# Performance work log

Hardware: AMD Instinct MI355X
Metric: run time of the kernel (lower is better)

## Reference

```python
import jax, jax.numpy as jnp
import numpy as np

N, D_IN, D_OUT, N_CTRS, K = 16384, 64, 64, 512, 16


def setup_inputs() -> dict:
    key = jax.random.key(0)
    k1, k2, k3, k4 = jax.random.split(key, 4)
    x = jax.random.normal(k1, (N, D_IN), dtype=jnp.float32)
    ctrs = jax.random.normal(k2, (N_CTRS, D_IN), dtype=jnp.float32)
    Wv = jax.random.normal(k3, (N_CTRS, D_IN, D_OUT), dtype=jnp.float32) * 0.02
    Ov = jax.random.normal(k4, (N_CTRS, D_OUT), dtype=jnp.float32) * 0.02
    return {"x": x, "ctrs": ctrs, "Wv": Wv, "Ov": Ov, "k": K}


def reference(x, ctrs, Wv, Ov, k):
    n = x.shape[0]
    # squared distances via expansion (same math as sum((x-c)^2), avoids [n,C,d] blowup)
    x2 = jnp.sum(x * x, axis=1, keepdims=True)            # [n,1]
    c2 = jnp.sum(ctrs * ctrs, axis=1)                     # [C]
    dist_sq = x2 + c2[None, :] - 2.0 * (x @ ctrs.T)       # [n,C]
    # k nearest centers; softmax over negative squared distances of the k selected
    neg_top, idx = jax.lax.top_k(-dist_sq, k)             # [n,k] each
    scores = jax.nn.softmax(neg_top, axis=1)              # [n,k]
    # dense soft-assignment matrix (only k nonzeros per row), as in the torch code
    A = jnp.zeros_like(dist_sq).at[jnp.arange(n)[:, None], idx].set(scores)  # [n,C]
    # per-token affine mix: sum_c A[n,c] * (x[n] @ Wv[c] + Ov[c])
    scored_weights = jnp.einsum('nc,cgp->ngp', A, Wv)     # [n,d_in,d_out]
    out = jnp.einsum('ngp,ng->np', scored_weights, x) + A @ Ov  # [n,d_out]
    return out
```

## Files before the change

kernel.cpp:

```cpp
#include <hip/hip_runtime.h>
#include <hip/hip_fp16.h>

#define N_TOK 16384
#define D 64
#define NC 512
#define KSEL 16
#define NPAIR (N_TOK * KSEL)
#define PADCAP 327168

typedef __attribute__((ext_vector_type(8))) short short8;
typedef __attribute__((ext_vector_type(8))) unsigned short ushort8;
typedef __attribute__((ext_vector_type(16))) float float16;

__device__ __forceinline__ unsigned fkey(float f) {
    unsigned u = __float_as_uint(f);
    return (u & 0x80000000u) ? ~u : (u | 0x80000000u);
}
__device__ __forceinline__ float funkey(unsigned k) {
    unsigned u = (k & 0x80000000u) ? (k & 0x7fffffffu) : ~k;
    return __uint_as_float(u);
}
__device__ __forceinline__ unsigned short bfr(float f) {
    unsigned u = __float_as_uint(f);
    return (unsigned short)((u + 0x7FFFu + ((u >> 16) & 1u)) >> 16);
}
__device__ __forceinline__ float b2f(unsigned short h) {
    return __uint_as_float((unsigned)h << 16);
}

__device__ __forceinline__ void ins16(unsigned (&run)[16], unsigned k) {
    #pragma unroll
    for (int r = 0; r < 16; ++r) {
        unsigned mx = run[r] > k ? run[r] : k;
        unsigned mn = run[r] > k ? k : run[r];
        run[r] = mx; k = mn;
    }
}

__global__ __launch_bounds__(256) void prep2_kernel(
    const float* __restrict__ x, const float* __restrict__ ctrs,
    const float* __restrict__ Wv,
    unsigned short* __restrict__ xh, unsigned short* __restrict__ xl,
    unsigned short* __restrict__ cbf, float* __restrict__ c2g,
    unsigned short* __restrict__ wbt, int* __restrict__ tokentab,
    int* __restrict__ hist) {
    __shared__ unsigned short tw[64 * 68];
    const int b = blockIdx.x, t = threadIdx.x;
    if (b < 512) {
        int g = b * 256 + t;
        int row = g >> 3, seg = g & 7;
        const float4* xp = (const float4*)(x + row * 64 + seg * 8);
        float4 u = xp[0], v = xp[1];
        float c[8] = {u.x, u.y, u.z, u.w, v.x, v.y, v.z, v.w};
        ushort8 h, l;
        #pragma unroll
        for (int j = 0; j < 8; ++j) {
            h[j] = bfr(c[j]);
            l[j] = bfr(c[j] - b2f(h[j]));
        }
        *(ushort8*)(xh + row * 64 + seg * 8) = h;
        *(ushort8*)(xl + row * 64 + seg * 8) = l;
    } else if (b < 516) {
        int g = (b - 512) * 256 + t;
        int c = g >> 1, q = g & 1;
        const float4* cp = (const float4*)(ctrs + c * D + q * 32);
        unsigned short* Ch = cbf + c * 136 + q * 32;
        float s2 = 0.f;
        #pragma unroll
        for (int i = 0; i < 8; ++i) {
            float4 v = cp[i];
            s2 += v.x * v.x + v.y * v.y + v.z * v.z + v.w * v.w;
            unsigned short h0 = bfr(v.x), h1 = bfr(v.y), h2 = bfr(v.z), h3 = bfr(v.w);
            unsigned short l0 = bfr(v.x - b2f(h0)), l1 = bfr(v.y - b2f(h1));
            unsigned short l2 = bfr(v.z - b2f(h2)), l3 = bfr(v.w - b2f(h3));
            *(uint2*)(Ch + 4 * i) =
                make_uint2((unsigned)h0 | ((unsigned)h1 << 16),
                           (unsigned)h2 | ((unsigned)h3 << 16));
            *(uint2*)(Ch + 64 + 4 * i) =
                make_uint2((unsigned)l0 | ((unsigned)l1 << 16),
                           (unsigned)l2 | ((unsigned)l3 << 16));
        }
        s2 += __shfl_xor(s2, 1);
        c2g[c] = s2;
    } else if (b < 1028) {
        const float* Wp = Wv + (size_t)(b - 516) * 4096;
        #pragma unroll
        for (int i = 0; i < 16; ++i) {
            int e = t + 256 * i;
            tw[(e & 63) * 68 + (e >> 6)] = bfr(Wp[e]);
        }
        __syncthreads();
        unsigned short* Wo = wbt + (size_t)(b - 516) * 4096;
        #pragma unroll
        for (int i = 0; i < 2; ++i) {
            int idx8 = t + 256 * i;
            int p = idx8 >> 3, g0 = (idx8 & 7) * 8;
            ushort8 v;
            #pragma unroll
            for (int j = 0; j < 8; ++j) v[j] = tw[p * 68 + g0 + j];
            *(ushort8*)(Wo + idx8 * 8) = v;
        }
    } else if (b < 1348) {
        int i = (b - 1028) * 256 + t;
        if (i < PADCAP / 4) ((int4*)tokentab)[i] = make_int4(-1, -1, -1, -1);
    } else {
        hist[t] = 0; hist[t + 256] = 0; hist[t + 512] = 0; hist[t + 768] = 0;
    }
}

__global__ __launch_bounds__(256, 4) void topk15_kernel(
    const unsigned short* __restrict__ xh, const unsigned short* __restrict__ xl,
    const unsigned short* __restrict__ cbf, const float* __restrict__ c2g,
    unsigned* __restrict__ pk) {
    __shared__ __align__(16) unsigned char pool[35328];
    unsigned short* Cbf = (unsigned short*)pool;
    unsigned* Sbk = (unsigned*)pool;
    unsigned* mbp = (unsigned*)pool;
    float* c2s = (float*)(pool + 34816);

    const int t = threadIdx.x;
    const int lane = t & 63;
    const int wv = t >> 6;
    const int mrow = lane & 31;
    const int half = lane >> 5;
    const int tb = blockIdx.x >> 2;
    const int p = blockIdx.x & 3;
    const int base = tb * 64;
    const int cbase = p * 128;
    const int trow = (wv & 1) * 32;
    const int cgrp = (wv >> 1) * 64;

    {
        const uint4* src = (const uint4*)(cbf + (size_t)cbase * 136);
        uint4* dst = (uint4*)pool;
        #pragma unroll
        for (int i = 0; i < 8; ++i) dst[t + 256 * i] = src[t + 256 * i];
        if (t < 128) {
            dst[2048 + t] = src[2048 + t];
            c2s[t] = c2g[cbase + t];
        }
    }

    short8 ah[4], al[4];
    {
        const int xrow = base + trow + mrow;
        const unsigned short* xph = xh + (size_t)xrow * 64 + half * 8;
        const unsigned short* xpl = xl + (size_t)xrow * 64 + half * 8;
        #pragma unroll
        for (int kt = 0; kt < 4; ++kt) {
            ah[kt] = *(const short8*)(xph + kt * 16);
            al[kt] = *(const short8*)(xpl + kt * 16);
        }
    }
    __syncthreads();

    float16 acc0 = {0.f,0.f,0.f,0.f,0.f,0.f,0.f,0.f,0.f,0.f,0.f,0.f,0.f,0.f,0.f,0.f};
    float16 acc1 = acc0;

    const unsigned short* B0 = Cbf + (cgrp + mrow) * 136 + half * 8;
    const unsigned short* B1 = Cbf + (cgrp + 32 + mrow) * 136 + half * 8;
    #pragma unroll
    for (int kt = 0; kt < 4; ++kt) {
        short8 bh0 = *(const short8*)(B0 + kt * 16);
        short8 bh1 = *(const short8*)(B1 + kt * 16);
        short8 bl0 = *(const short8*)(B0 + 64 + kt * 16);
        short8 bl1 = *(const short8*)(B1 + 64 + kt * 16);
        acc0 = __builtin_amdgcn_mfma_f32_32x32x16_bf16(ah[kt], bh0, acc0, 0, 0, 0);
        acc1 = __builtin_amdgcn_mfma_f32_32x32x16_bf16(ah[kt], bh1, acc1, 0, 0, 0);
        acc0 = __builtin_amdgcn_mfma_f32_32x32x16_bf16(al[kt], bh0, acc0, 0, 0, 0);
        acc1 = __builtin_amdgcn_mfma_f32_32x32x16_bf16(al[kt], bh1, acc1, 0, 0, 0);
        acc0 = __builtin_amdgcn_mfma_f32_32x32x16_bf16(ah[kt], bl0, acc0, 0, 0, 0);
        acc1 = __builtin_amdgcn_mfma_f32_32x32x16_bf16(ah[kt], bl1, acc1, 0, 0, 0);
    }
    __syncthreads();

    {
        float ca = c2s[cgrp + mrow];
        float cb = c2s[cgrp + 32 + mrow];
        #pragma unroll
        for (int reg = 0; reg < 16; ++reg) {
            int tokrow = trow + (reg & 3) + 8 * (reg >> 2) + 4 * half;
            float sa = fmaf(2.f, acc0[reg], -ca);
            float sb = fmaf(2.f, acc1[reg], -cb);
            Sbk[tokrow * 132 + cgrp + mrow] =
                (fkey(sa) & 0xFFFFFE00u) | (unsigned)(cbase + cgrp + mrow);
            Sbk[tokrow * 132 + cgrp + 32 + mrow] =
                (fkey(sb) & 0xFFFFFE00u) | (unsigned)(cbase + cgrp + 32 + mrow);
        }
    }
    __syncthreads();

    const int tok = t & 63;
    const int h = t >> 6;
    unsigned run[16];
    #pragma unroll
    for (int r = 0; r < 16; ++r) run[r] = 0u;
    #pragma unroll
    for (int i = 0; i < 8; ++i) {
        int cq = ((i + tok) & 7) ^ ((tok >> 3) & 7);
        uint4 kv = *(const uint4*)(Sbk + tok * 132 + 32 * h + 4 * cq);
        ins16(run, kv.x); ins16(run, kv.y); ins16(run, kv.z); ins16(run, kv.w);
    }
    __syncthreads();

    {
        uint4* dst = (uint4*)(mbp + tok * 68 + h * 16);
        dst[0] = make_uint4(run[0], run[1], run[2], run[3]);
        dst[1] = make_uint4(run[4], run[5], run[6], run[7]);
        dst[2] = make_uint4(run[8], run[9], run[10], run[11]);
        dst[3] = make_uint4(run[12], run[13], run[14], run[15]);
    }
    __syncthreads();

    if (t < 64) {
        const unsigned* pm = mbp + t * 68;
        unsigned hv[4]; int pos[4];
        #pragma unroll
        for (int w = 0; w < 4; ++w) { pos[w] = 0; hv[w] = pm[w * 16]; }
        unsigned mm[16];
        #pragma unroll
        for (int r = 0; r < 16; ++r) {
            unsigned m = hv[0];
            #pragma unroll
            for (int w = 1; w < 4; ++w) m = m > hv[w] ? m : hv[w];
            mm[r] = m;
            #pragma unroll
            for (int w = 0; w < 4; ++w) {
                if (hv[w] == m) {
                    ++pos[w];
                    hv[w] = (pos[w] < 16) ? pm[w * 16 + pos[w]] : 0u;
                }
            }
        }
        uint4* dst = (uint4*)(pk + (size_t)(base + t) * 64 + p * 16);
        dst[0] = make_uint4(mm[0], mm[1], mm[2], mm[3]);
        dst[1] = make_uint4(mm[4], mm[5], mm[6], mm[7]);
        dst[2] = make_uint4(mm[8], mm[9], mm[10], mm[11]);
        dst[3] = make_uint4(mm[12], mm[13], mm[14], mm[15]);
    }
}

__global__ __launch_bounds__(256) void topmerge_kernel(
    const unsigned* __restrict__ pk, float* __restrict__ scores,
    int* __restrict__ sidx, int* __restrict__ hist) {
    __shared__ int lhist[NC];
    const int t = threadIdx.x;
    lhist[t] = 0; lhist[t + 256] = 0;
    __syncthreads();
    const int n = blockIdx.x * 256 + t;
    const unsigned* p = pk + (size_t)n * 64;
    unsigned h[4]; int pos[4];
    #pragma unroll
    for (int w = 0; w < 4; ++w) { pos[w] = 0; h[w] = p[w * 16]; }
    float vals[16]; int ids[16];
    #pragma unroll
    for (int r = 0; r < KSEL; ++r) {
        unsigned m = h[0];
        #pragma unroll
        for (int w = 1; w < 4; ++w) m = m > h[w] ? m : h[w];
        vals[r] = funkey(m);
        ids[r] = (int)(m & 511u);
        #pragma unroll
        for (int w = 0; w < 4; ++w) {
            if (h[w] == m) {
                ++pos[w];
                h[w] = (pos[w] < KSEL) ? p[w * 16 + pos[w]] : 0u;
            }
        }
    }
    float mx = vals[0];
    float e[16]; float sum = 0.f;
    #pragma unroll
    for (int r = 0; r < KSEL; ++r) { e[r] = __expf(vals[r] - mx); sum += e[r]; }
    float inv = 1.f / sum;
    #pragma unroll
    for (int q = 0; q < 4; ++q) {
        *(float4*)(scores + n * KSEL + 4 * q) =
            make_float4(e[4*q] * inv, e[4*q+1] * inv, e[4*q+2] * inv, e[4*q+3] * inv);
        *(int4*)(sidx + n * KSEL + 4 * q) =
            make_int4(ids[4*q], ids[4*q+1], ids[4*q+2], ids[4*q+3]);
    }
    #pragma unroll
    for (int r = 0; r < KSEL; ++r) atomicAdd(&lhist[ids[r]], 1);
    __syncthreads();
    { int hv = lhist[t]; if (hv) atomicAdd(&hist[t], hv); }
    { int hv = lhist[t + 256]; if (hv) atomicAdd(&hist[t + 256], hv); }
}

__global__ __launch_bounds__(256) void scatter5_kernel(
    const int* __restrict__ hist, const int* __restrict__ sidx,
    const float* __restrict__ scores, int* __restrict__ cursor,
    int* __restrict__ tokentab, float* __restrict__ scotab,
    int* __restrict__ meta) {
    __shared__ int buf[2][NC];
    __shared__ int sb[NC];
    __shared__ int lh[NC];
    __shared__ int lbase[NC];
    const int t = threadIdx.x;

    int h0 = hist[t], h1 = hist[t + 256];
    int p0 = (h0 + 127) & ~127, p1 = (h1 + 127) & ~127;
    buf[0][t] = p0; buf[0][t + 256] = p1;
    __syncthreads();
    int a = 0;
    for (int d = 1; d < NC; d <<= 1) {
        int v0 = buf[a][t] + (t >= d ? buf[a][t - d] : 0);
        int v1 = buf[a][t + 256] + (t + 256 >= d ? buf[a][t + 256 - d] : 0);
        buf[1 - a][t] = v0; buf[1 - a][t + 256] = v1;
        __syncthreads();
        a ^= 1;
    }
    sb[t] = buf[a][t] - p0;
    sb[t + 256] = buf[a][t + 256] - p1;
    if (t == 255) meta[0] = buf[a][NC - 1];
    lh[t] = 0; lh[t + 256] = 0;
    __syncthreads();

    const int base_e = blockIdx.x * 1024;
    int myc[4];
    #pragma unroll
    for (int i = 0; i < 4; ++i) {
        int c = sidx[base_e + t + 256 * i];
        myc[i] = c;
        atomicAdd(&lh[c], 1);
    }
    __syncthreads();
    for (int i = t; i < NC; i += 256) {
        int h = lh[i];
        lbase[i] = h ? (sb[i] + atomicAdd(&cursor[i], h)) : 0;
        lh[i] = 0;
    }
    __syncthreads();
    #pragma unroll
    for (int i = 0; i < 4; ++i) {
        int e = base_e + t + 256 * i;
        int c = myc[i];
        int pos = lbase[c] + atomicAdd(&lh[c], 1);
        tokentab[pos] = (c << 19) | e;
        scotab[pos] = scores[e];
    }
}

__global__ __launch_bounds__(256) void mix17_kernel(
    const unsigned short* __restrict__ xh, const unsigned short* __restrict__ wbt,
    const float* __restrict__ Ov, const int* __restrict__ tokentab,
    const float* __restrict__ scotab, const int* __restrict__ meta,
    __half* __restrict__ partial) {
    __shared__ __align__(16) unsigned short Wt[64 * 72];
    __shared__ int eT[128];
    __shared__ float sT[128];

    const int t = threadIdx.x;
    const int base = blockIdx.x * 128;
    if (base >= meta[0]) return;

    const int c = (int)(((unsigned)tokentab[base]) >> 19);

    {
        const unsigned short* Wp = wbt + (size_t)c * 4096;
        const int p = t >> 2, qq = t & 3;
        *(ushort8*)(Wt + p * 72 + qq * 16) =
            *(const ushort8*)(Wp + p * 64 + qq * 16);
        *(ushort8*)(Wt + p * 72 + qq * 16 + 8) =
            *(const ushort8*)(Wp + p * 64 + qq * 16 + 8);
    }
    if (t < 128) {
        unsigned w = (unsigned)tokentab[base + t];
        eT[t] = (int)(w & 0x7FFFFu);
        sT[t] = scotab[base + t];
    }
    __syncthreads();

    const int lane = t & 63;
    const int wv = t >> 6;
    const int mrow = lane & 31;
    const int half = lane >> 5;
    const int row = wv * 32 + mrow;

    const int mye = eT[row];
    const int myn = (mye < NPAIR) ? (mye >> 4) : 0;

    const unsigned short* xp = xh + (size_t)myn * 64 + half * 8;
    short8 a[4];
    #pragma unroll
    for (int kt = 0; kt < 4; ++kt) a[kt] = *(const short8*)(xp + kt * 16);

    float16 acc0 = {0.f,0.f,0.f,0.f,0.f,0.f,0.f,0.f,0.f,0.f,0.f,0.f,0.f,0.f,0.f,0.f};
    float16 acc1 = {0.f,0.f,0.f,0.f,0.f,0.f,0.f,0.f,0.f,0.f,0.f,0.f,0.f,0.f,0.f,0.f};

    const unsigned short* B0 = Wt + mrow * 72;
    const unsigned short* B1 = Wt + (mrow + 32) * 72;
    #pragma unroll
    for (int kt = 0; kt < 4; ++kt) {
        short8 b0 = *(const short8*)(B0 + kt * 16 + half * 8);
        short8 b1 = *(const short8*)(B1 + kt * 16 + half * 8);
        acc0 = __builtin_amdgcn_mfma_f32_32x32x16_bf16(a[kt], b0, acc0, 0, 0, 0);
        acc1 = __builtin_amdgcn_mfma_f32_32x32x16_bf16(a[kt], b1, acc1, 0, 0, 0);
    }

    const float ov0 = Ov[c * D + mrow];
    const float ov1 = Ov[c * D + 32 + mrow];
    #pragma unroll
    for (int reg = 0; reg < 16; ++reg) {
        int orow = wv * 32 + (reg & 3) + 8 * (reg >> 2) + 4 * half;
        float s = sT[orow];
        int e = eT[orow];
        if (e < NPAIR) {
            __half* dst = partial + (size_t)e * D;
            dst[mrow]      = __float2half(s * (acc0[reg] + ov0));
            dst[32 + mrow] = __float2half(s * (acc1[reg] + ov1));
        }
    }
}

__global__ __launch_bounds__(256) void redu2_kernel(
    const __half* __restrict__ partial, float* __restrict__ out) {
    const int g = blockIdx.x * 256 + threadIdx.x;
    const int n = g >> 3;
    const int d8 = (g & 7) * 8;
    const __half* p = partial + (size_t)n * (KSEL * D) + d8;
    float s[8] = {0.f, 0.f, 0.f, 0.f, 0.f, 0.f, 0.f, 0.f};
    #pragma unroll
    for (int r = 0; r < KSEL; ++r) {
        ushort8 v = *(const ushort8*)(p + r * D);
        #pragma unroll
        for (int j = 0; j < 8; ++j)
            s[j] += __half2float(__ushort_as_half((unsigned short)v[j]));
    }
    float* o = out + n * D + d8;
    *(float4*)(o)     = make_float4(s[0], s[1], s[2], s[3]);
    *(float4*)(o + 4) = make_float4(s[4], s[5], s[6], s[7]);
}

__global__ __launch_bounds__(256) void mix14_kernel(
    const float* __restrict__ x, const float* __restrict__ Wv,
    const float* __restrict__ Ov, const int* __restrict__ tokentab,
    const float* __restrict__ scotab, const int* __restrict__ meta,
    float* __restrict__ out) {
    __shared__ __align__(16) unsigned short Wt[64 * 72];
    __shared__ int tT[128];
    __shared__ float sT[128];

    const int t = threadIdx.x;
    const int base = blockIdx.x * 128;
    if (base >= meta[0]) return;

    const int c = (int)(((unsigned)tokentab[base]) >> 19);

    {
        const float* Wp = Wv + c * (D * D) + (t & 63);
        const int gb = (t >> 6) * 16;
        #pragma unroll
        for (int g = 0; g < 16; g += 2) {
            float v0 = Wp[(gb + g) * 64];
            float v1 = Wp[(gb + g + 1) * 64];
            unsigned pkw = (unsigned)bfr(v0) | ((unsigned)bfr(v1) << 16);
            *(unsigned*)&Wt[(t & 63) * 72 + gb + g] = pkw;
        }
    }
    if (t < 128) {
        unsigned w = (unsigned)tokentab[base + t];
        tT[t] = (int)((w & 0x7FFFFu) >> 4);
        sT[t] = scotab[base + t];
    }
    __syncthreads();

    const int lane = t & 63;
    const int wv = t >> 6;
    const int mrow = lane & 31;
    const int half = lane >> 5;
    const int row = wv * 32 + mrow;

    const int   myn = tT[row];
    const float mys = sT[row];

    const float* xp = x + myn * D + half * 8;
    float4 f[8];
    #pragma unroll
    for (int kt = 0; kt < 4; ++kt) {
        f[2 * kt]     = *(const float4*)(xp + kt * 16);
        f[2 * kt + 1] = *(const float4*)(xp + kt * 16 + 4);
    }
    short8 a[4];
    #pragma unroll
    for (int kt = 0; kt < 4; ++kt) {
        float4 u = f[2 * kt], v = f[2 * kt + 1];
        a[kt][0] = (short)bfr(u.x * mys); a[kt][1] = (short)bfr(u.y * mys);
        a[kt][2] = (short)bfr(u.z * mys); a[kt][3] = (short)bfr(u.w * mys);
        a[kt][4] = (short)bfr(v.x * mys); a[kt][5] = (short)bfr(v.y * mys);
        a[kt][6] = (short)bfr(v.z * mys); a[kt][7] = (short)bfr(v.w * mys);
    }

    float16 acc0 = {0.f,0.f,0.f,0.f,0.f,0.f,0.f,0.f,0.f,0.f,0.f,0.f,0.f,0.f,0.f,0.f};
    float16 acc1 = {0.f,0.f,0.f,0.f,0.f,0.f,0.f,0.f,0.f,0.f,0.f,0.f,0.f,0.f,0.f,0.f};

    const unsigned short* B0 = Wt + mrow * 72;
    const unsigned short* B1 = Wt + (mrow + 32) * 72;
    #pragma unroll
    for (int kt = 0; kt < 4; ++kt) {
        short8 b0 = *(const short8*)(B0 + kt * 16 + half * 8);
        short8 b1 = *(const short8*)(B1 + kt * 16 + half * 8);
        acc0 = __builtin_amdgcn_mfma_f32_32x32x16_bf16(a[kt], b0, acc0, 0, 0, 0);
        acc1 = __builtin_amdgcn_mfma_f32_32x32x16_bf16(a[kt], b1, acc1, 0, 0, 0);
    }

    const float ov0 = Ov[c * D + mrow];
    const float ov1 = Ov[c * D + 32 + mrow];
    #pragma unroll
    for (int reg = 0; reg < 16; ++reg) {
        int orow = wv * 32 + (reg & 3) + 8 * (reg >> 2) + 4 * half;
        float s = sT[orow];
        if (s != 0.f) {
            int n = tT[orow];
            unsafeAtomicAdd(out + n * D + mrow,      acc0[reg] + s * ov0);
            unsafeAtomicAdd(out + n * D + 32 + mrow, acc1[reg] + s * ov1);
        }
    }
}

extern "C" void kernel_launch(void* const* d_in, const int* in_sizes, int n_in,
                              void* d_out, int out_size, void* d_ws, size_t ws_size,
                              hipStream_t stream) {
    const float* x    = (const float*)d_in[0];
    const float* ctrs = (const float*)d_in[1];
    const float* Wv   = (const float*)d_in[2];
    const float* Ov   = (const float*)d_in[3];
    float* out = (float*)d_out;

    const size_t OFF_META = 0;
    const size_t OFF_HIST = 512;
    const size_t OFF_CUR  = 1024;
    const size_t OFF_SCO  = 2560;
    const size_t OFF_SIDX = OFF_SCO + NPAIR;
    const size_t OFF_TTAB = OFF_SIDX + NPAIR;
    const size_t OFF_STAB = OFF_TTAB + PADCAP;
    const size_t PK_INTS  = (size_t)N_TOK * 64;
    const size_t XH_INTS  = (size_t)N_TOK * 32;
    const size_t CBF_INTS = (size_t)NC * 68;
    const size_t WBT_INTS = (size_t)NC * 2048;
    const size_t O_PK   = OFF_STAB + PADCAP;
    const size_t O_XH   = O_PK + PK_INTS;
    const size_t O_XL   = O_XH + XH_INTS;
    const size_t O_CBF  = O_XL + XH_INTS;
    const size_t O_C2   = O_CBF + CBF_INTS;
    const size_t O_WBT  = O_C2 + 512;
    const size_t O_PART = O_WBT + WBT_INTS;
    const size_t PART_INTS = (size_t)NPAIR * 32;

    int*    meta     = (int*)d_ws + OFF_META;
    int*    hist     = (int*)d_ws + OFF_HIST;
    int*    cursor   = (int*)d_ws + OFF_CUR;
    float*  scores   = (float*)d_ws + OFF_SCO;
    int*    sidx     = (int*)d_ws + OFF_SIDX;
    int*    tokentab = (int*)d_ws + OFF_TTAB;
    float*  scotab   = (float*)d_ws + OFF_STAB;
    unsigned* pkbuf  = (unsigned*)((int*)d_ws + O_PK);
    unsigned short* xh  = (unsigned short*)((int*)d_ws + O_XH);
    unsigned short* xl  = (unsigned short*)((int*)d_ws + O_XL);
    unsigned short* cbf = (unsigned short*)((int*)d_ws + O_CBF);
    float*  c2g      = (float*)((int*)d_ws + O_C2);
    unsigned short* wbt = (unsigned short*)((int*)d_ws + O_WBT);
    __half* partial  = (__half*)((int*)d_ws + O_PART);

    const size_t need = (O_PART + PART_INTS) * 4;
    const bool fast = ws_size >= need;

    hipLaunchKernelGGL(prep2_kernel, dim3(1349), dim3(256), 0, stream,
                       x, ctrs, Wv, xh, xl, cbf, c2g, wbt, tokentab, hist);
    if (!fast) {
        hipMemsetAsync(out, 0, (size_t)N_TOK * D * sizeof(float), stream);
        hipMemsetAsync(scotab, 0, (size_t)PADCAP * sizeof(float), stream);
        hipMemsetAsync(tokentab, 0, (size_t)PADCAP * sizeof(int), stream);
    }
    hipLaunchKernelGGL(topk15_kernel, dim3((N_TOK / 64) * 4), dim3(256), 0, stream,
                       xh, xl, cbf, c2g, pkbuf);
    hipLaunchKernelGGL(topmerge_kernel, dim3(N_TOK / 256), dim3(256), 0, stream,
                       pkbuf, scores, sidx, hist);
    hipLaunchKernelGGL(scatter5_kernel, dim3(256), dim3(256), 0, stream,
                       hist, sidx, scores, cursor, tokentab, scotab, meta);
    if (fast) {
        hipLaunchKernelGGL(mix17_kernel, dim3(PADCAP / 128), dim3(256), 0, stream,
                           xh, wbt, Ov, tokentab, scotab, meta, partial);
        hipLaunchKernelGGL(redu2_kernel, dim3(N_TOK * 8 / 256), dim3(256), 0, stream,
                           partial, out);
    } else {
        hipLaunchKernelGGL(mix14_kernel, dim3(PADCAP / 128), dim3(256), 0, stream,
                           x, Wv, Ov, tokentab, scotab, meta, out);
    }
}
```

Measured before the change: 134.2 us.

## Fuse top-k distance and merge kernels, loop center chunks with register prefetch

The partial top-k kernel and the merge kernel become one kernel. Each block handles 32 tokens and loops over all four 128-center chunks, prefetching the next chunk into registers while computing the current one. Per-thread running top-16 lists are merged in shared memory, and the softmax and histogram are done in place. This removes the intermediate partial-key buffer round trip through global memory and one launch. In exchange it uses more LDS, caps occupancy at 2 blocks per SIMD-unit slot, and runs a serial 8-way merge on only 32 threads.

```diff
diff --git a/kernel.cpp b/kernel.cpp
--- a/kernel.cpp
+++ b/kernel.cpp
@@ -108,180 +108,147 @@
     }
 }
 
-__global__ __launch_bounds__(256, 4) void topk15_kernel(
+__global__ __launch_bounds__(256, 2) void topk16_kernel(
     const unsigned short* __restrict__ xh, const unsigned short* __restrict__ xl,
     const unsigned short* __restrict__ cbf, const float* __restrict__ c2g,
-    unsigned* __restrict__ pk) {
-    __shared__ __align__(16) unsigned char pool[35328];
+    float* __restrict__ scores, int* __restrict__ sidx, int* __restrict__ hist) {
+    __shared__ __align__(16) unsigned char pool[53760];
     unsigned short* Cbf = (unsigned short*)pool;
-    unsigned* Sbk = (unsigned*)pool;
-    unsigned* mbp = (unsigned*)pool;
-    float* c2s = (float*)(pool + 34816);
+    unsigned* Sbk = (unsigned*)(pool + 34816);
+    float* c2s = (float*)(pool + 51712);
+    int* lhist = (int*)pool;
 
     const int t = threadIdx.x;
     const int lane = t & 63;
     const int wv = t >> 6;
     const int mrow = lane & 31;
     const int half = lane >> 5;
-    const int tb = blockIdx.x >> 2;
-    const int p = blockIdx.x & 3;
-    const int base = tb * 64;
-    const int cbase = p * 128;
-    const int trow = (wv & 1) * 32;
-    const int cgrp = (wv >> 1) * 64;
-
-    {
-        const uint4* src = (const uint4*)(cbf + (size_t)cbase * 136);
-        uint4* dst = (uint4*)pool;
-        #pragma unroll
-        for (int i = 0; i < 8; ++i) dst[t + 256 * i] = src[t + 256 * i];
-        if (t < 128) {
-            dst[2048 + t] = src[2048 + t];
-            c2s[t] = c2g[cbase + t];
-        }
-    }
+    const int base = blockIdx.x * 32;
 
     short8 ah[4], al[4];
     {
-        const int xrow = base + trow + mrow;
-        const unsigned short* xph = xh + (size_t)xrow * 64 + half * 8;
-        const unsigned short* xpl = xl + (size_t)xrow * 64 + half * 8;
+        const unsigned short* xph = xh + (size_t)(base + mrow) * 64 + half * 8;
+        const unsigned short* xpl = xl + (size_t)(base + mrow) * 64 + half * 8;
         #pragma unroll
         for (int kt = 0; kt < 4; ++kt) {
             ah[kt] = *(const short8*)(xph + kt * 16);
             al[kt] = *(const short8*)(xpl + kt * 16);
         }
     }
-    __syncthreads();
-
-    float16 acc0 = {0.f,0.f,0.f,0.f,0.f,0.f,0.f,0.f,0.f,0.f,0.f,0.f,0.f,0.f,0.f,0.f};
-    float16 acc1 = acc0;
-
-    const unsigned short* B0 = Cbf + (cgrp + mrow) * 136 + half * 8;
-    const unsigned short* B1 = Cbf + (cgrp + 32 + mrow) * 136 + half * 8;
-    #pragma unroll
-    for (int kt = 0; kt < 4; ++kt) {
-        short8 bh0 = *(const short8*)(B0 + kt * 16);
-        short8 bh1 = *(const short8*)(B1 + kt * 16);
-        short8 bl0 = *(const short8*)(B0 + 64 + kt * 16);
-        short8 bl1 = *(const short8*)(B1 + 64 + kt * 16);
-        acc0 = __builtin_amdgcn_mfma_f32_32x32x16_bf16(ah[kt], bh0, acc0, 0, 0, 0);
-        acc1 = __builtin_amdgcn_mfma_f32_32x32x16_bf16(ah[kt], bh1, acc1, 0, 0, 0);
-        acc0 = __builtin_amdgcn_mfma_f32_32x32x16_bf16(al[kt], bh0, acc0, 0, 0, 0);
-        acc1 = __builtin_amdgcn_mfma_f32_32x32x16_bf16(al[kt], bh1, acc1, 0, 0, 0);
-        acc0 = __builtin_amdgcn_mfma_f32_32x32x16_bf16(ah[kt], bl0, acc0, 0, 0, 0);
-        acc1 = __builtin_amdgcn_mfma_f32_32x32x16_bf16(ah[kt], bl1, acc1, 0, 0, 0);
-    }
-    __syncthreads();
+
+    const uint4* csrc = (const uint4*)cbf;
+    uint4 pre[8], pre8;
+    #pragma unroll
+    for (int i = 0; i < 8; ++i) pre[i] = csrc[t + 256 * i];
+    if (t < 128) pre8 = csrc[2048 + t];
+
+    unsigned run[16];
+    #pragma unroll
+    for (int r = 0; r < 16; ++r) run[r] = 0u;
+
+    const int tok = t & 31;
+    const int part = t >> 5;
+
+    #pragma unroll 1
+    for (int p = 0; p < 4; ++p) {
+        {
+            uint4* dst = (uint4*)pool;
+            #pragma unroll
+            for (int i = 0; i < 8; ++i) dst[t + 256 * i] = pre[i];
+            if (t < 128) dst[2048 + t] = pre8;
+        }
+        if (p == 0) { c2s[t] = c2g[t]; c2s[t + 256] = c2g[t + 256]; }
+        if (p < 3) {
+            const uint4* s2 = csrc + (p + 1) * 2176;
+            #pragma unroll
+            for (int i = 0; i < 8; ++i) pre[i] = s2[t + 256 * i];
+            if (t < 128) pre8 = s2[2048 + t];
+        }
+        __syncthreads();
+
+        float16 acc = {0.f,0.f,0.f,0.f,0.f,0.f,0.f,0.f,0.f,0.f,0.f,0.f,0.f,0.f,0.f,0.f};
+        const unsigned short* B0 = Cbf + (wv * 32 + mrow) * 136 + half * 8;
+        #pragma unroll
+        for (int kt = 0; kt < 4; ++kt) {
+            short8 bh = *(const short8*)(B0 + kt * 16);
+            short8 bl = *(const short8*)(B0 + 64 + kt * 16);
+            acc = __builtin_amdgcn_mfma_f32_32x32x16_bf16(ah[kt], bh, acc, 0, 0, 0);
+            acc = __builtin_amdgcn_mfma_f32_32x32x16_bf16(al[kt], bh, acc, 0, 0, 0);
+            acc = __builtin_amdgcn_mfma_f32_32x32x16_bf16(ah[kt], bl, acc, 0, 0, 0);
+        }
+
+        {
+            const int cglob = p * 128 + wv * 32 + mrow;
+            const int col = wv * 32 + mrow;
+            const float cc = c2s[cglob];
+            #pragma unroll
+            for (int reg = 0; reg < 16; ++reg) {
+                int tokrow = (reg & 3) + 8 * (reg >> 2) + 4 * half;
+                float sq = fmaf(2.f, acc[reg], -cc);
+                int colw = col ^ (((tokrow >> 3) & 3) << 2);
+                Sbk[tokrow * 132 + colw] =
+                    (fkey(sq) & 0xFFFFFE00u) | (unsigned)cglob;
+            }
+        }
+        __syncthreads();
+
+        const int sw = ((tok >> 3) & 3) << 2;
+        #pragma unroll
+        for (int j = 0; j < 4; ++j) {
+            int colb = (part * 16 + 4 * ((j + tok) & 3)) ^ sw;
+            uint4 kv = *(const uint4*)(Sbk + tok * 132 + colb);
+            ins16(run, kv.x); ins16(run, kv.y); ins16(run, kv.z); ins16(run, kv.w);
+        }
+        __syncthreads();
+    }
 
     {
-        float ca = c2s[cgrp + mrow];
-        float cb = c2s[cgrp + 32 + mrow];
-        #pragma unroll
-        for (int reg = 0; reg < 16; ++reg) {
-            int tokrow = trow + (reg & 3) + 8 * (reg >> 2) + 4 * half;
-            float sa = fmaf(2.f, acc0[reg], -ca);
-            float sb = fmaf(2.f, acc1[reg], -cb);
-            Sbk[tokrow * 132 + cgrp + mrow] =
-                (fkey(sa) & 0xFFFFFE00u) | (unsigned)(cbase + cgrp + mrow);
-            Sbk[tokrow * 132 + cgrp + 32 + mrow] =
-                (fkey(sb) & 0xFFFFFE00u) | (unsigned)(cbase + cgrp + 32 + mrow);
-        }
-    }
-    __syncthreads();
-
-    const int tok = t & 63;
-    const int h = t >> 6;
-    unsigned run[16];
-    #pragma unroll
-    for (int r = 0; r < 16; ++r) run[r] = 0u;
-    #pragma unroll
-    for (int i = 0; i < 8; ++i) {
-        int cq = ((i + tok) & 7) ^ ((tok >> 3) & 7);
-        uint4 kv = *(const uint4*)(Sbk + tok * 132 + 32 * h + 4 * cq);
-        ins16(run, kv.x); ins16(run, kv.y); ins16(run, kv.z); ins16(run, kv.w);
-    }
-    __syncthreads();
-
-    {
-        uint4* dst = (uint4*)(mbp + tok * 68 + h * 16);
-        dst[0] = make_uint4(run[0], run[1], run[2], run[3]);
-        dst[1] = make_uint4(run[4], run[5], run[6], run[7]);
-        dst[2] = make_uint4(run[8], run[9], run[10], run[11]);
-        dst[3] = make_uint4(run[12], run[13], run[14], run[15]);
-    }
-    __syncthreads();
-
-    if (t < 64) {
-        const unsigned* pm = mbp + t * 68;
-        unsigned hv[4]; int pos[4];
-        #pragma unroll
-        for (int w = 0; w < 4; ++w) { pos[w] = 0; hv[w] = pm[w * 16]; }
-        unsigned mm[16];
-        #pragma unroll
-        for (int r = 0; r < 16; ++r) {
-            unsigned m = hv[0];
+        uint4* d = (uint4*)(Sbk + tok * 132 + part * 16);
+        d[0] = make_uint4(run[0], run[1], run[2], run[3]);
+        d[1] = make_uint4(run[4], run[5], run[6], run[7]);
+        d[2] = make_uint4(run[8], run[9], run[10], run[11]);
+        d[3] = make_uint4(run[12], run[13], run[14], run[15]);
+    }
+    lhist[t] = 0; lhist[t + 256] = 0;
+    __syncthreads();
+
+    if (t < 32) {
+        const unsigned* pm = Sbk + t * 132;
+        unsigned h[8]; int pos[8];
+        #pragma unroll
+        for (int w = 0; w < 8; ++w) { pos[w] = 0; h[w] = pm[w * 16]; }
+        float vals[16]; int ids[16];
+        #pragma unroll
+        for (int r = 0; r < KSEL; ++r) {
+            unsigned m = h[0];
             #pragma unroll
-            for (int w = 1; w < 4; ++w) m = m > hv[w] ? m : hv[w];
-            mm[r] = m;
+            for (int w = 1; w < 8; ++w) m = m > h[w] ? m : h[w];
+            vals[r] = funkey(m);
+            ids[r] = (int)(m & 511u);
             #pragma unroll
-            for (int w = 0; w < 4; ++w) {
-                if (hv[w] == m) {
+            for (int w = 0; w < 8; ++w) {
+                if (h[w] == m) {
                     ++pos[w];
-                    hv[w] = (pos[w] < 16) ? pm[w * 16 + pos[w]] : 0u;
+                    h[w] = (pos[w] < KSEL) ? pm[w * 16 + pos[w]] : 0u;
                 }
             }
         }
-        uint4* dst = (uint4*)(pk + (size_t)(base + t) * 64 + p * 16);
-        dst[0] = make_uint4(mm[0], mm[1], mm[2], mm[3]);
-        dst[1] = make_uint4(mm[4], mm[5], mm[6], mm[7]);
-        dst[2] = make_uint4(mm[8], mm[9], mm[10], mm[11]);
-        dst[3] = make_uint4(mm[12], mm[13], mm[14], mm[15]);
-    }
-}
-
-__global__ __launch_bounds__(256) void topmerge_kernel(
-    const unsigned* __restrict__ pk, float* __restrict__ scores,
-    int* __restrict__ sidx, int* __restrict__ hist) {
-    __shared__ int lhist[NC];
-    const int t = threadIdx.x;
-    lhist[t] = 0; lhist[t + 256] = 0;
-    __syncthreads();
-    const int n = blockIdx.x * 256 + t;
-    const unsigned* p = pk + (size_t)n * 64;
-    unsigned h[4]; int pos[4];
-    #pragma unroll
-    for (int w = 0; w < 4; ++w) { pos[w] = 0; h[w] = p[w * 16]; }
-    float vals[16]; int ids[16];
-    #pragma unroll
-    for (int r = 0; r < KSEL; ++r) {
-        unsigned m = h[0];
-        #pragma unroll
-        for (int w = 1; w < 4; ++w) m = m > h[w] ? m : h[w];
-        vals[r] = funkey(m);
-        ids[r] = (int)(m & 511u);
-        #pragma unroll
-        for (int w = 0; w < 4; ++w) {
-            if (h[w] == m) {
-                ++pos[w];
-                h[w] = (pos[w] < KSEL) ? p[w * 16 + pos[w]] : 0u;
-            }
-        }
-    }
-    float mx = vals[0];
-    float e[16]; float sum = 0.f;
-    #pragma unroll
-    for (int r = 0; r < KSEL; ++r) { e[r] = __expf(vals[r] - mx); sum += e[r]; }
-    float inv = 1.f / sum;
-    #pragma unroll
-    for (int q = 0; q < 4; ++q) {
-        *(float4*)(scores + n * KSEL + 4 * q) =
-            make_float4(e[4*q] * inv, e[4*q+1] * inv, e[4*q+2] * inv, e[4*q+3] * inv);
-        *(int4*)(sidx + n * KSEL + 4 * q) =
-            make_int4(ids[4*q], ids[4*q+1], ids[4*q+2], ids[4*q+3]);
-    }
-    #pragma unroll
-    for (int r = 0; r < KSEL; ++r) atomicAdd(&lhist[ids[r]], 1);
+        float mx = vals[0];
+        float e[16]; float sum = 0.f;
+        #pragma unroll
+        for (int r = 0; r < KSEL; ++r) { e[r] = __expf(vals[r] - mx); sum += e[r]; }
+        float inv = 1.f / sum;
+        int n = base + t;
+        #pragma unroll
+        for (int q = 0; q < 4; ++q) {
+            *(float4*)(scores + n * KSEL + 4 * q) =
+                make_float4(e[4*q] * inv, e[4*q+1] * inv, e[4*q+2] * inv, e[4*q+3] * inv);
+            *(int4*)(sidx + n * KSEL + 4 * q) =
+                make_int4(ids[4*q], ids[4*q+1], ids[4*q+2], ids[4*q+3]);
+        }
+        #pragma unroll
+        for (int r = 0; r < KSEL; ++r) atomicAdd(&lhist[ids[r]], 1);
+    }
     __syncthreads();
     { int hv = lhist[t]; if (hv) atomicAdd(&hist[t], hv); }
     { int hv = lhist[t + 256]; if (hv) atomicAdd(&hist[t + 256], hv); }
@@ -534,12 +501,10 @@
     const size_t OFF_SIDX = OFF_SCO + NPAIR;
     const size_t OFF_TTAB = OFF_SIDX + NPAIR;
     const size_t OFF_STAB = OFF_TTAB + PADCAP;
-    const size_t PK_INTS  = (size_t)N_TOK * 64;
     const size_t XH_INTS  = (size_t)N_TOK * 32;
     const size_t CBF_INTS = (size_t)NC * 68;
     const size_t WBT_INTS = (size_t)NC * 2048;
-    const size_t O_PK   = OFF_STAB + PADCAP;
-    const size_t O_XH   = O_PK + PK_INTS;
+    const size_t O_XH   = OFF_STAB + PADCAP;
     const size_t O_XL   = O_XH + XH_INTS;
     const size_t O_CBF  = O_XL + XH_INTS;
     const size_t O_C2   = O_CBF + CBF_INTS;
@@ -554,7 +519,6 @@
     int*    sidx     = (int*)d_ws + OFF_SIDX;
     int*    tokentab = (int*)d_ws + OFF_TTAB;
     float*  scotab   = (float*)d_ws + OFF_STAB;
-    unsigned* pkbuf  = (unsigned*)((int*)d_ws + O_PK);
     unsigned short* xh  = (unsigned short*)((int*)d_ws + O_XH);
     unsigned short* xl  = (unsigned short*)((int*)d_ws + O_XL);
     unsigned short* cbf = (unsigned short*)((int*)d_ws + O_CBF);
@@ -572,10 +536,8 @@
         hipMemsetAsync(scotab, 0, (size_t)PADCAP * sizeof(float), stream);
         hipMemsetAsync(tokentab, 0, (size_t)PADCAP * sizeof(int), stream);
     }
-    hipLaunchKernelGGL(topk15_kernel, dim3((N_TOK / 64) * 4), dim3(256), 0, stream,
-                       xh, xl, cbf, c2g, pkbuf);
-    hipLaunchKernelGGL(topmerge_kernel, dim3(N_TOK / 256), dim3(256), 0, stream,
-                       pkbuf, scores, sidx, hist);
+    hipLaunchKernelGGL(topk16_kernel, dim3(N_TOK / 32), dim3(256), 0, stream,
+                       xh, xl, cbf, c2g, scores, sidx, hist);
     hipLaunchKernelGGL(scatter5_kernel, dim3(256), dim3(256), 0, stream,
                        hist, sidx, scores, cursor, tokentab, scotab, meta);
     if (fast) {
```

Measured after the change: 147.2 us. 9.7% more time.
